# Performance work log

Hardware: AMD Instinct MI355X
Metric: run time of the kernel (lower is better)

## Reference

```python
import jax, jax.numpy as jnp
import numpy as np

B, NEG = 2, 16            # queries, negatives per query
N, E, D = 10000, 80000, 128  # nodes, edges, feature dim (in_dim == out_dim)
NUM_REL = 237
L = 3                     # PNA layers
NODE_RATIO = 0.1
K = max(1, int(NODE_RATIO * N))  # static top-k: every repeated graph has exactly N nodes
EPS = 1e-5


def _score(hidden, rel, lin_W, lin_b, m1_W, m1_b, m2_W, m2_b):
    heur = jnp.concatenate([hidden, rel], axis=-1) @ lin_W + lin_b
    x = heur * hidden
    h = jax.nn.relu(x @ m1_W + m1_b)
    return jnp.squeeze(h @ m2_W + m2_b, -1)


def _pna_conv(hidden, src, dst, emask, deg, pre_W, pre_b, post_W, post_b, out_W, out_b):
    """PNA layer with mean/max/min/std aggregators and identity/amplification/attenuation
    scalers, restricted to edges where emask is True. deg is the (clamped >=1) degree used
    by the scalers."""
    BN = hidden.shape[0]
    # message: pre-linear on [x_i (target), x_j (source)] per edge  -> (Erep, D)
    m = jnp.concatenate([hidden[dst], hidden[src]], axis=-1) @ pre_W + pre_b
    w = emask.astype(hidden.dtype)[:, None]
    cnt = jax.ops.segment_sum(emask.astype(hidden.dtype), dst, num_segments=BN)
    denom = jnp.maximum(cnt, 1.0)[:, None]
    s1 = jax.ops.segment_sum(m * w, dst, num_segments=BN)
    s2 = jax.ops.segment_sum(m * m * w, dst, num_segments=BN)
    mean = s1 / denom
    var = jax.nn.relu(s2 / denom - mean * mean)
    std = jnp.sqrt(var + EPS)
    has = (cnt > 0)[:, None]
    mx = jnp.where(has, jax.ops.segment_max(jnp.where(emask[:, None], m, -jnp.inf), dst, num_segments=BN), 0.0)
    mn = jnp.where(has, jax.ops.segment_min(jnp.where(emask[:, None], m, jnp.inf), dst, num_segments=BN), 0.0)
    agg = jnp.concatenate([mean, mx, mn, std], axis=-1)           # (BN, 4D)
    logd = jnp.log(deg + 1.0)                                     # deg >= 1 -> logd > 0
    avg_log = jnp.mean(logd)
    agg = jnp.concatenate([agg, agg * (logd / avg_log)[:, None], agg * (avg_log / logd)[:, None]], axis=-1)  # (BN, 12D)
    return (agg @ post_W + post_b) @ out_W + out_b


def _forward(h_index, r_index, t_index, hidden_states, edge_index, rel_embedding,
             lin_W, lin_b, m1_W, m1_b, m2_W, m2_b, pre_W, pre_b, post_W, post_b, out_W, out_b):
    sc = (lin_W, lin_b, m1_W, m1_b, m2_W, m2_b)
    # negative_sample_to_tail
    is_t_neg = jnp.all(h_index == h_index[:, :1], axis=-1, keepdims=True)
    h_idx = jnp.where(is_t_neg, h_index, t_index)
    t_idx = jnp.where(is_t_neg, t_index, h_index)
    r_idx = jnp.where(is_t_neg, r_index, r_index + NUM_REL)
    # repeat_graph
    offsets = jnp.arange(B, dtype=h_idx.dtype) * N               # (B,)
    src = jnp.tile(edge_index[0], B) + jnp.repeat(offsets, E)    # (B*E,)
    dst = jnp.tile(edge_index[1], B) + jnp.repeat(offsets, E)
    BN = B * N
    rel_embeds = rel_embedding[r_idx[:, 0]].astype(hidden_states.dtype)  # (B, D)
    flat_h = h_idx[:, 0] + offsets
    flat_t = t_idx[:, 0] + offsets
    # literal `repeat_interleave(N, dim=0)[:B]` quirk -> row arange(B)//N of gathered embs
    sel = jnp.arange(B) // N
    h_vals = hidden_states[h_idx[:, 0]][sel]                     # (B, D)
    t_vals = hidden_states[t_idx[:, 0]][sel]
    # init_input_embeds: boundary condition + initial score at head nodes
    boundary = jnp.zeros((BN, D), hidden_states.dtype).at[flat_t].set(t_vals).at[flat_h].set(h_vals)
    score = jnp.zeros(BN, jnp.float32).at[flat_h].set(_score(h_vals, rel_embeds, *sc))
    hidden = boundary
    rel_per_node = jnp.repeat(rel_embeds, N, axis=0)             # (BN, D), rel_embeds[batch_rep]
    rows = jnp.arange(B)[:, None]
    for l in range(L):
        # select_edges_pyg with degree_ratio=1.0: all out-edges of per-graph top-k nodes
        _, idx = jax.lax.top_k(score.reshape(B, N), K)           # (B, K)
        node_sel = jnp.zeros((B, N), bool).at[rows, idx].set(True).reshape(-1)
        emask = node_sel[src]                                    # (B*E,) selected-edge mask
        out_deg = jax.ops.segment_sum(emask.astype(jnp.float32), src, num_segments=BN)
        deg_sub = jnp.maximum(out_deg.astype(hidden.dtype), 1.0)
        new_hidden = _pna_conv(hidden, src, dst, emask, deg_sub,
                               pre_W[l], pre_b[l], post_W[l], post_b[l], out_W[l], out_b[l])
        # residual only for nodes with selected outgoing edges
        hidden = jnp.where((out_deg > 0)[:, None], hidden + new_hidden, hidden)
        score = _score(hidden, rel_per_node, *sc)
    # read out scores at (repeated) tail indices -> (B, NEG)
    return score[t_idx + offsets[:, None]]


def setup_inputs() -> dict:
    key = jax.random.key(0)
    ks = jax.random.split(key, 14)
    s = 0.05
    hi = jax.random.randint(ks[0], (B, 1), 0, N)
    h_index = jnp.tile(hi, (1, NEG))                 # constant per row (assert in forward)
    r0 = jax.random.randint(ks[1], (B, 1), 0, NUM_REL)
    r_index = jnp.tile(r0, (1, NEG))                 # constant per row (assert in forward)
    t_index = jax.random.randint(ks[2], (B, NEG), 0, N)
    hidden_states = jax.random.normal(ks[3], (N, D), jnp.float32)
    edge_index = jax.random.randint(ks[4], (2, E), 0, N)
    return {
        "h_index": h_index, "r_index": r_index, "t_index": t_index,
        "hidden_states": hidden_states, "edge_index": edge_index,
        "rel_embedding": jax.random.normal(ks[5], (2 * NUM_REL, D), jnp.float32) * s,
        "lin_W": jax.random.normal(ks[6], (2 * D, D), jnp.float32) * s, "lin_b": jnp.zeros(D, jnp.float32),
        "m1_W": jax.random.normal(ks[7], (D, D), jnp.float32) * s, "m1_b": jnp.zeros(D, jnp.float32),
        "m2_W": jax.random.normal(ks[8], (D, 1), jnp.float32) * s, "m2_b": jnp.zeros(1, jnp.float32),
        "pre_W": jax.random.normal(ks[9], (L, 2 * D, D), jnp.float32) * s, "pre_b": jnp.zeros((L, D), jnp.float32),
        "post_W": jax.random.normal(ks[10], (L, 12 * D, D), jnp.float32) * s, "post_b": jnp.zeros((L, D), jnp.float32),
        "out_W": jax.random.normal(ks[11], (L, D, D), jnp.float32) * s, "out_b": jnp.zeros((L, D), jnp.float32),
    }


def reference(h_index, r_index, t_index, hidden_states, edge_index, rel_embedding,
              lin_W, lin_b, m1_W, m1_b, m2_W, m2_b, pre_W, pre_b, post_W, post_b, out_W, out_b):
    return _forward(h_index, r_index, t_index, hidden_states, edge_index, rel_embedding,
                    lin_W, lin_b, m1_W, m1_b, m2_W, m2_b, pre_W, pre_b, post_W, post_b, out_W, out_b)
```

## Files before the change

kernel.cpp:

```cpp
#include <hip/hip_runtime.h>
#include <math.h>

#define Bq 2
#define NEG 16
#define Nn 10000
#define Ee 80000
#define Dd 128
#define NUM_REL 237
#define Ll 3
#define K_SEL 1000
#define BN (Bq*Nn)
#define EPSV 1e-5f
#define MAXACT 2048
#define MAXTOUCH 8192
#define SELCAP 3328
#define LN2F 0.69314718056f

constexpr size_t HID_OFF   = 0;
constexpr size_t SCORE_OFF = HID_OFF   + (size_t)BN*Dd*4;
constexpr size_t CVEC_OFF  = SCORE_OFF + (size_t)BN*4;
constexpr size_t HDR_OFF   = CVEC_OFF  + (size_t)Bq*Dd*4;
constexpr size_t THR_OFF   = HDR_OFF   + 64*4;
constexpr size_t INC_OFF   = THR_OFF   + Bq*8;
constexpr size_t DEG_OFF   = INC_OFF   + (size_t)BN*4;
constexpr size_t SLOT_OFF  = DEG_OFF   + (size_t)BN*4;
constexpr size_t CNT_OFF   = SLOT_OFF  + (size_t)BN*4;
constexpr size_t SDEG_OFF  = CNT_OFF   + (size_t)MAXACT*4;
constexpr size_t S1_OFF    = SDEG_OFF  + (size_t)MAXACT*4;
constexpr size_t S2_OFF    = S1_OFF    + (size_t)MAXACT*Dd*4;
constexpr size_t MXB_OFF   = S2_OFF    + (size_t)MAXACT*Dd*4;
constexpr size_t MNB_OFF   = MXB_OFF   + (size_t)MAXACT*Dd*4;
constexpr size_t TPART_OFF = MNB_OFF   + (size_t)MAXACT*Dd*4;
constexpr size_t ALIST_OFF = TPART_OFF + (size_t)4*MAXACT*Dd*4;
constexpr size_t FLAG_OFF  = ALIST_OFF + (size_t)MAXACT*4;
constexpr size_t TLIST_OFF = FLAG_OFF  + (size_t)BN*4;
constexpr size_t EDGE_OFF  = TLIST_OFF + (size_t)MAXTOUCH*4;
constexpr size_t CTR_OFF   = EDGE_OFF  + (size_t)Bq*Ee*2*4;

__device__ __forceinline__ unsigned encf(float f){
  unsigned u = __float_as_uint(f);
  return (u & 0x80000000u) ? ~u : (u | 0x80000000u);
}
__device__ __forceinline__ float decf(unsigned e){
  unsigned u = (e & 0x80000000u) ? (e & 0x7FFFFFFFu) : ~e;
  return __uint_as_float(u);
}
__device__ __forceinline__ unsigned long long make_key(float f, int i){
  unsigned d = ~encf(f);
  return ((unsigned long long)d << 32) | (unsigned)i;
}

__global__ __launch_bounds__(256) void k_init(
    const int* __restrict__ h_index, const int* __restrict__ r_index, const int* __restrict__ t_index,
    const float* __restrict__ hidden_states, const float* __restrict__ rel_embedding,
    const float* __restrict__ lin_W, const float* __restrict__ lin_b,
    const float* __restrict__ m1_W, const float* __restrict__ m1_b,
    const float* __restrict__ m2_W, const float* __restrict__ m2_b,
    int* __restrict__ hdr, float* __restrict__ cvec, float* __restrict__ hidden,
    float* __restrict__ score, unsigned* __restrict__ flag, int* __restrict__ tlist,
    unsigned* __restrict__ deg0, unsigned* __restrict__ ctr)
{
  __shared__ struct {
    int hbuf[Bq*NEG], tbuf[Bq*NEG], rbuf[Bq*NEG];
    int fh[Bq], ft[Bq], r0[Bq], eqf[Bq], hsrc, tsrc;
    float s0red[Dd]; float sc0;
    float relv[Bq][Dd], cv[Bq][Dd], hv[Dd], x[Bq][Dd], p[Bq][Dd];
  } sp;
  const int tid = threadIdx.x;
  const int bid = blockIdx.x;
  if (tid < Bq*NEG){
    sp.hbuf[tid] = h_index[tid];
    sp.tbuf[tid] = t_index[tid];
    sp.rbuf[tid] = r_index[tid];
  }
  if (tid < Dd) sp.s0red[tid] = fmaxf(m1_b[tid], 0.f) * m2_W[tid];
  __syncthreads();
  if (tid == 0){
    for (int b = 0; b < Bq; b++){
      bool eq = true;
      for (int j = 1; j < NEG; j++) eq = eq && (sp.hbuf[b*NEG+j] == sp.hbuf[b*NEG]);
      int h0 = eq ? sp.hbuf[b*NEG] : sp.tbuf[b*NEG];
      int t0 = eq ? sp.tbuf[b*NEG] : sp.hbuf[b*NEG];
      int r0 = eq ? sp.rbuf[b*NEG] : sp.rbuf[b*NEG] + NUM_REL;
      sp.fh[b] = h0 + b*Nn; sp.ft[b] = t0 + b*Nn;
      sp.r0[b] = r0; sp.eqf[b] = eq ? 1 : 0;
      if (b == 0){ sp.hsrc = h0; sp.tsrc = t0; }
    }
    float s = m2_b[0];
    for (int k = 0; k < Dd; k++) s += sp.s0red[k];
    sp.sc0 = s;
    if (bid == 0){
      ctr[4] = __float_as_uint(s);
      hdr[0] = sp.fh[0]; hdr[1] = sp.fh[1];
      hdr[2] = sp.ft[0]; hdr[3] = sp.ft[1];
      for (int b = 0; b < Bq; b++)
        for (int j = 0; j < NEG; j++){
          int tj = sp.eqf[b] ? sp.tbuf[b*NEG+j] : sp.hbuf[b*NEG+j];
          hdr[4 + b*NEG + j] = tj + b*Nn;
        }
      int cand[4] = { sp.ft[0], sp.fh[0], sp.ft[1], sp.fh[1] };
      int n = 0;
      for (int c = 0; c < 4; c++){
        bool dup = false;
        for (int m = 0; m < n; m++) dup = dup || (tlist[m] == cand[c]);
        if (!dup) tlist[n++] = cand[c];
        flag[cand[c]] = 1u;
      }
      ctr[3] = (unsigned)n;
    }
  }
  __syncthreads();
  const int fh0 = sp.fh[0], fh1 = sp.fh[1];
  const int ft0 = sp.ft[0], ft1 = sp.ft[1];
  const float sc0 = sp.sc0;
  if (bid == 0){
    int b = tid >> 7, d = tid & 127;
    sp.relv[b][d] = rel_embedding[(size_t)sp.r0[b]*Dd + d];
    if (b == 0) sp.hv[d] = hidden_states[(size_t)sp.hsrc*Dd + d];
    __syncthreads();
    float acc = lin_b[d];
    #pragma unroll 8
    for (int k = 0; k < Dd; k++) acc += sp.relv[b][k]*lin_W[(Dd+k)*Dd + d];
    sp.cv[b][d] = acc; cvec[b*Dd + d] = acc;
    hidden[(size_t)sp.ft[b]*Dd + d] = hidden_states[(size_t)sp.tsrc*Dd + d];
    hidden[(size_t)sp.fh[b]*Dd + d] = hidden_states[(size_t)sp.hsrc*Dd + d];
    __syncthreads();
    float hv = sp.hv[d];
    float heur = sp.cv[b][d];
    #pragma unroll 8
    for (int k = 0; k < Dd; k++) heur += sp.hv[k]*lin_W[k*Dd + d];
    sp.x[b][d] = heur * hv;
    __syncthreads();
    float a2 = m1_b[d];
    #pragma unroll 8
    for (int k = 0; k < Dd; k++) a2 += sp.x[b][k]*m1_W[k*Dd + d];
    sp.p[b][d] = fmaxf(a2, 0.f) * m2_W[d];
    __syncthreads();
    if (tid < Bq){
      float s = m2_b[0];
      for (int k = 0; k < Dd; k++) s += sp.p[tid][k];
      score[sp.fh[tid]] = s;
    }
  } else {
    int zb = bid - 1, znb = gridDim.x - 1;
    int zt = zb*256 + tid, zs = znb*256;
    float4 z4 = make_float4(0.f, 0.f, 0.f, 0.f);
    for (int i = zt; i < BN*32; i += zs){
      int row = i >> 5;
      if (row != ft0 && row != ft1 && row != fh0 && row != fh1)
        ((float4*)hidden)[i] = z4;
    }
    for (int v = zt; v < BN; v += zs){
      if (v != ft0 && v != ft1 && v != fh0 && v != fh1) flag[v] = 0u;
      if (v != fh0 && v != fh1) score[v] = sc0;
      if (v < Nn) deg0[v] = 0u;
    }
  }
}

__global__ __launch_bounds__(256) void k_selzero(
    const float* __restrict__ score, const int* __restrict__ tlist,
    unsigned long long* __restrict__ thr,
    float* __restrict__ s1, float* __restrict__ s2,
    unsigned* __restrict__ mxb, unsigned* __restrict__ mnb,
    unsigned* __restrict__ incnt, unsigned* __restrict__ ctr,
    const int* __restrict__ ei, unsigned* __restrict__ deg0, int do_deg0)
{
  int tid = threadIdx.x;
  int bid = blockIdx.x;
  if (bid < Bq){
    int b = bid;
    int nt = (int)ctr[3];
    unsigned d0 = ~encf(__uint_as_float(ctr[4]));
    __shared__ unsigned sd[SELCAP];
    __shared__ unsigned short sidx[SELCAP];
    __shared__ unsigned hist[256], histT[256];
    __shared__ int ntb_sh;
    __shared__ unsigned long long pref_sh;
    __shared__ unsigned kk_sh;
    if (tid == 0){ ntb_sh = 0; pref_sh = 0ull; kk_sh = K_SEL; }
    __syncthreads();
    int vlo = b*Nn, vhi = vlo + Nn;
    for (int i = tid; i < nt; i += 256){
      int v = tlist[i];
      if (v >= vlo && v < vhi){
        int pos = atomicAdd(&ntb_sh, 1);
        if (pos < SELCAP){
          sd[pos] = ~encf(score[v]);
          sidx[pos] = (unsigned short)(v - vlo);
        }
      }
    }
    __syncthreads();
    int ntb = min(ntb_sh, SELCAP);
    unsigned nvirt = (unsigned)(Nn - ntb);
    for (int pass = 7; pass >= 0; --pass){
      hist[tid] = 0u; histT[tid] = 0u;
      __syncthreads();
      unsigned long long pref = pref_sh;
      int sh_hi = 8*(pass+1);
      for (int j = tid; j < ntb; j += 256){
        unsigned long long key = ((unsigned long long)sd[j] << 32) | (unsigned long long)sidx[j];
        bool ok = (pass==7) || ((key >> sh_hi) == (pref >> sh_hi));
        if (ok) atomicAdd(&hist[(unsigned)(key >> (8*pass)) & 255u], 1u);
        if (pass < 4){
          unsigned idx = sidx[j];
          bool oki = (pass == 3) || ((idx >> sh_hi) == (((unsigned)pref) >> sh_hi));
          if (oki) atomicAdd(&histT[(idx >> (8*pass)) & 255u], 1u);
        }
      }
      __syncthreads();
      if (pass >= 4){
        if (tid == 0){
          unsigned long long keyv_hi = ((unsigned long long)d0 << 32);
          bool ok = (pass==7) || ((keyv_hi >> sh_hi) == (pref_sh >> sh_hi));
          if (ok) atomicAdd(&hist[(d0 >> (8*(pass-4))) & 255u], nvirt);
        }
      } else {
        if ((unsigned)(pref >> 32) == d0){
          unsigned long long hf = 0ull;
          if (pass < 3) hf = (unsigned long long)((((unsigned)pref) >> sh_hi)) << sh_hi;
          unsigned long long lo = hf + ((unsigned long long)tid << (8*pass));
          unsigned long long hi = lo + (1ull << (8*pass));
          unsigned long long nn = (unsigned long long)Nn;
          unsigned long long l2 = lo < nn ? lo : nn;
          unsigned long long h2 = hi < nn ? hi : nn;
          if (h2 > l2){
            unsigned c = (unsigned)(h2 - l2) - histT[tid];
            if (c > 0u) atomicAdd(&hist[tid], c);
          }
        }
      }
      __syncthreads();
      {
        unsigned kk = kk_sh;
        unsigned cum = 0;
        for (int i = 0; i < tid; i++) cum += hist[i];
        unsigned h = hist[tid];
        if (h > 0u && cum < kk && kk <= cum + h){
          pref_sh |= ((unsigned long long)tid) << (8*pass);
          kk_sh = kk - cum;
        }
      }
      __syncthreads();
    }
    if (tid == 0) thr[b] = pref_sh;
  } else {
    int zb = bid - Bq, znb = gridDim.x - Bq;
    int zt = zb*256 + tid, zs = znb*256;
    for (int i = zt; i < MAXACT*Dd; i += zs){
      s1[i] = 0.f; s2[i] = 0.f; mxb[i] = 0u; mnb[i] = 0xFFFFFFFFu;
    }
    for (int i = zt; i < BN; i += zs) incnt[i] = 0u;
    if (zt < 3) ctr[zt] = 0u;
    if (do_deg0){
      for (int e = zt; e < Ee; e += zs) atomicAdd(&deg0[ei[e]], 1u);
    }
  }
}

__global__ void k_build(const int* __restrict__ ei, const float* __restrict__ score,
                        const unsigned long long* __restrict__ thr,
                        const unsigned* __restrict__ deg0,
                        int* __restrict__ node_slot, int* __restrict__ alist,
                        float* __restrict__ slot_deg, unsigned* __restrict__ incnt,
                        int* __restrict__ edges, unsigned* __restrict__ ctr,
                        unsigned* __restrict__ flag, int* __restrict__ tlist){
  int i = blockIdx.x*blockDim.x + threadIdx.x;
  unsigned long long th0 = thr[0], th1 = thr[1];
  if (i < BN){
    int b = (i >= Nn) ? 1 : 0;
    int v0 = i - b*Nn;
    unsigned dg = deg0[v0];
    if (dg > 0u && make_key(score[i], v0) <= (b ? th1 : th0)){
      int slot = (int)atomicAdd(&ctr[0], 1u);
      alist[slot] = i; node_slot[i] = slot; slot_deg[slot] = (float)dg;
      atomicAdd((float*)&ctr[2], logf((float)dg + 1.0f));
      if (atomicExch(&flag[i], 1u) == 0u){
        int p = (int)atomicAdd(&ctr[3], 1u);
        tlist[p] = i;
      }
    }
  }
  if (i < Ee){
    int s0 = ei[i], d0e = ei[Ee + i];
    unsigned dgd = deg0[d0e];
    if (make_key(score[s0], s0) <= th0 && dgd > 0u && make_key(score[d0e], d0e) <= th0){
      int j = (int)atomicAdd(&ctr[1], 1u);
      edges[2*j] = s0; edges[2*j+1] = d0e;
      atomicAdd(&incnt[d0e], 1u);
    }
    int sv = s0 + Nn, dv = d0e + Nn;
    if (make_key(score[sv], s0) <= th1 && dgd > 0u && make_key(score[dv], d0e) <= th1){
      int j = (int)atomicAdd(&ctr[1], 1u);
      edges[2*j] = sv; edges[2*j+1] = dv;
      atomicAdd(&incnt[dv], 1u);
    }
  }
}

__global__ __launch_bounds__(256) void k_messages(
    const float* __restrict__ hidden, const int* __restrict__ edges,
    const int* __restrict__ node_slot,
    const float* __restrict__ preW, const float* __restrict__ preb,
    float* __restrict__ s1, float* __restrict__ s2,
    unsigned* __restrict__ mxb, unsigned* __restrict__ mnb,
    const unsigned* __restrict__ ctr){
  int ne = (int)ctr[1];
  int tid = threadIdx.x;
  int half = tid >> 7, d = tid & 127;
  __shared__ float sd[8][Dd], ss[8][Dd];
  float pb = preb[d];
  for (int j0 = blockIdx.x*8; j0 < ne; j0 += gridDim.x*8){
    int base = j0 + half*4;
    int nv = ne - base; if (nv > 4) nv = 4; if (nv < 0) nv = 0;
    int dsl[4];
    #pragma unroll
    for (int e = 0; e < 4; e++){
      int j = (e < nv) ? base + e : j0;
      int s = edges[2*j]; int dv = edges[2*j+1];
      dsl[e] = node_slot[dv];
      sd[half*4+e][d] = hidden[(size_t)dv*Dd + d];
      ss[half*4+e][d] = hidden[(size_t)s*Dd + d];
    }
    __syncthreads();
    float a[4] = {pb, pb, pb, pb};
    #pragma unroll 4
    for (int k = 0; k < Dd; k++){
      float w0 = preW[k*Dd + d];
      float w1 = preW[(Dd+k)*Dd + d];
      #pragma unroll
      for (int e = 0; e < 4; e++)
        a[e] += sd[half*4+e][k]*w0 + ss[half*4+e][k]*w1;
    }
    for (int e = 0; e < nv; e++){
      int dslot = dsl[e];
      atomicAdd(&s1[dslot*Dd + d], a[e]);
      atomicAdd(&s2[dslot*Dd + d], a[e]*a[e]);
      atomicMax(&mxb[dslot*Dd + d], encf(a[e]));
      atomicMin(&mnb[dslot*Dd + d], encf(a[e]));
    }
    __syncthreads();
  }
}

__global__ __launch_bounds__(512) void k_post(
    const unsigned* __restrict__ incnt, const int* __restrict__ alist,
    const float* __restrict__ s1, const float* __restrict__ s2,
    const unsigned* __restrict__ mxb, const unsigned* __restrict__ mnb,
    const float* __restrict__ slot_deg,
    const float* __restrict__ postW, float* __restrict__ tpart,
    const unsigned* __restrict__ ctr){
  int na = (int)ctr[0];
  int bid = blockIdx.x;
  int tile = bid & 63, ch = bid >> 6;
  if (tile*32 >= na) return;
  float logsum = __uint_as_float(ctr[2]);
  float avg = (logsum + (float)(BN - na)*LN2F) / (float)BN;
  __shared__ float lb[32*136];
  __shared__ float wbuf[3*16*128];
  __shared__ float sden[32];
  __shared__ unsigned shas[32];
  int tid = threadIdx.x;
  if (tid < 32){
    int slot = tile*32 + tid;
    unsigned c = (slot < na) ? incnt[alist[slot]] : 0u;
    sden[tid] = fmaxf((float)c, 1.0f);
    shas[tid] = c;
  }
  __syncthreads();
  for (int idx = tid; idx < 32*Dd; idx += 512){
    int sl = idx >> 7, kk = idx & 127;
    int gi = (tile*32 + sl)*Dd + kk;
    float den = sden[sl];
    float val;
    if (ch == 0)      val = s1[gi]/den;
    else if (ch == 1) val = shas[sl] ? decf(mxb[gi]) : 0.f;
    else if (ch == 2) val = shas[sl] ? decf(mnb[gi]) : 0.f;
    else {
      float mv = s1[gi]/den;
      float var = s2[gi]/den - mv*mv;
      val = sqrtf(fmaxf(var, 0.f) + EPSV);
    }
    lb[sl*136 + kk] = val;
  }
  int cg = tid & 31, rg = tid >> 5;
  int c0 = cg*4;
  float a0[2][4], a1[2][4], a2[2][4];
  #pragma unroll
  for (int i = 0; i < 2; i++)
    #pragma unroll
    for (int j = 0; j < 4; j++){ a0[i][j]=0.f; a1[i][j]=0.f; a2[i][j]=0.f; }
  for (int chunk = 0; chunk < 8; ++chunk){
    #pragma unroll
    for (int i = 0; i < 3; ++i){
      int f = tid + i*512;
      int q = f >> 9, r = f & 511;
      int kk = r >> 5, c4 = r & 31;
      int grow = q*512 + ch*128 + chunk*16 + kk;
      ((float4*)wbuf)[f] = *(const float4*)(postW + (size_t)grow*Dd + c4*4);
    }
    __syncthreads();
    #pragma unroll
    for (int k4 = 0; k4 < 4; ++k4){
      float4 av0 = *(const float4*)&lb[(rg*2+0)*136 + chunk*16 + k4*4];
      float4 av1 = *(const float4*)&lb[(rg*2+1)*136 + chunk*16 + k4*4];
      #pragma unroll
      for (int j = 0; j < 4; ++j){
        int kk = k4*4 + j;
        float4 w0 = *(const float4*)&wbuf[kk*128 + c0];
        float4 w1 = *(const float4*)&wbuf[(16+kk)*128 + c0];
        float4 w2 = *(const float4*)&wbuf[(32+kk)*128 + c0];
        float av[2] = { (&av0.x)[j], (&av1.x)[j] };
        #pragma unroll
        for (int i = 0; i < 2; i++){
          float a = av[i];
          a0[i][0] += a*w0.x; a0[i][1] += a*w0.y; a0[i][2] += a*w0.z; a0[i][3] += a*w0.w;
          a1[i][0] += a*w1.x; a1[i][1] += a*w1.y; a1[i][2] += a*w1.z; a1[i][3] += a*w1.w;
          a2[i][0] += a*w2.x; a2[i][1] += a*w2.y; a2[i][2] += a*w2.z; a2[i][3] += a*w2.w;
        }
      }
    }
    __syncthreads();
  }
  #pragma unroll
  for (int i = 0; i < 2; i++){
    int slot = tile*32 + rg*2 + i;
    if (slot < na){
      float dg = slot_deg[slot];
      float logd = logf(dg + 1.f);
      float al = logd/avg, be = avg/logd;
      float4 r;
      r.x = a0[i][0] + al*a1[i][0] + be*a2[i][0];
      r.y = a0[i][1] + al*a1[i][1] + be*a2[i][1];
      r.z = a0[i][2] + al*a1[i][2] + be*a2[i][2];
      r.w = a0[i][3] + al*a1[i][3] + be*a2[i][3];
      *(float4*)(tpart + (size_t)ch*MAXACT*Dd + (size_t)slot*Dd + c0) = r;
    }
  }
}

__global__ __launch_bounds__(256) void k_out_resid(
    const float* __restrict__ tpart, const int* __restrict__ alist,
    const float* __restrict__ outW, const float* __restrict__ outb,
    const float* __restrict__ postb, float* __restrict__ hidden,
    const unsigned* __restrict__ ctr){
  int na = (int)ctr[0];
  int tile = blockIdx.x;
  if (tile*32 >= na) return;
  __shared__ float tr[32*136];
  __shared__ float wbuf[16*128];
  int tid = threadIdx.x;
  for (int idx = tid; idx < 32*Dd; idx += 256){
    int sl = idx >> 7, kk = idx & 127;
    size_t o = (size_t)(tile*32 + sl)*Dd + kk;
    tr[sl*136 + kk] = tpart[o] + tpart[(size_t)MAXACT*Dd + o]
                    + tpart[(size_t)2*MAXACT*Dd + o] + tpart[(size_t)3*MAXACT*Dd + o]
                    + postb[kk];
  }
  int cg = tid & 31, rg = tid >> 5;
  int c0 = cg*4;
  float4 ob = *(const float4*)(outb + c0);
  float acc[4][4];
  #pragma unroll
  for (int r = 0; r < 4; r++){ acc[r][0]=ob.x; acc[r][1]=ob.y; acc[r][2]=ob.z; acc[r][3]=ob.w; }
  for (int chunk = 0; chunk < 8; ++chunk){
    #pragma unroll
    for (int i = 0; i < 2; ++i){
      int f = tid + i*256;
      int kk = f >> 5, c4 = f & 31;
      ((float4*)wbuf)[f] = *(const float4*)(outW + (size_t)(chunk*16 + kk)*Dd + c4*4);
    }
    __syncthreads();
    #pragma unroll
    for (int k4 = 0; k4 < 4; ++k4){
      float4 av[4];
      #pragma unroll
      for (int r = 0; r < 4; r++)
        av[r] = *(const float4*)&tr[(rg*4+r)*136 + chunk*16 + k4*4];
      #pragma unroll
      for (int j = 0; j < 4; ++j){
        float4 w = *(const float4*)&wbuf[(k4*4+j)*128 + c0];
        #pragma unroll
        for (int r = 0; r < 4; r++){
          float a = (&av[r].x)[j];
          acc[r][0] += a*w.x; acc[r][1] += a*w.y; acc[r][2] += a*w.z; acc[r][3] += a*w.w;
        }
      }
    }
    __syncthreads();
  }
  #pragma unroll
  for (int r = 0; r < 4; r++){
    int slot = tile*32 + rg*4 + r;
    if (slot < na){
      int v = alist[slot];
      float* hp = hidden + (size_t)v*Dd + c0;
      float4 h4 = *(float4*)hp;
      h4.x += acc[r][0]; h4.y += acc[r][1]; h4.z += acc[r][2]; h4.w += acc[r][3];
      *(float4*)hp = h4;
    }
  }
}

__global__ __launch_bounds__(256) void k_score(
    const float* __restrict__ hidden, const float* __restrict__ cvec,
    const float* __restrict__ linW,
    const float* __restrict__ m1W, const float* __restrict__ m1b,
    const float* __restrict__ m2W, const float* __restrict__ m2b,
    const int* __restrict__ tlist, const unsigned* __restrict__ ctr,
    float* __restrict__ score,
    const int* __restrict__ ovr, int ovr_n, float* __restrict__ outp){
  int nt = (ovr_n > 0) ? ovr_n : (int)ctr[3];
  const int* list = (ovr_n > 0) ? ovr : tlist;
  int nb = blockIdx.x * 32;
  if (nb >= nt) return;
  __shared__ float sh[32*Dd];
  __shared__ float sx[32*Dd];
  __shared__ float sc[2*Dd];
  __shared__ int   sv[32];
  __shared__ float red[32*33];
  int tid = threadIdx.x;
  if (tid < 32){
    int idx = nb + tid;
    sv[tid] = (idx < nt) ? list[idx] : list[nb];
  }
  sc[tid] = cvec[tid];
  __syncthreads();
  for (int q = tid; q < 32*32; q += 256){
    int row = q >> 5, f4 = q & 31;
    ((float4*)sh)[row*32 + f4] = ((const float4*)(hidden + (size_t)sv[row]*Dd))[f4];
  }
  __syncthreads();
  int cg = tid & 31, rg = tid >> 5;
  int c0 = cg*4;
  float acc[4][4];
  #pragma unroll
  for (int i = 0; i < 4; i++){ acc[i][0]=0.f; acc[i][1]=0.f; acc[i][2]=0.f; acc[i][3]=0.f; }
  for (int k4 = 0; k4 < 32; k4++){
    float4 av[4];
    #pragma unroll
    for (int i = 0; i < 4; i++) av[i] = ((float4*)sh)[(rg*4+i)*32 + k4];
    #pragma unroll
    for (int j = 0; j < 4; j++){
      float4 w = *(const float4*)(linW + (size_t)(k4*4+j)*Dd + c0);
      #pragma unroll
      for (int i = 0; i < 4; i++){
        float a = (&av[i].x)[j];
        acc[i][0] += a*w.x; acc[i][1] += a*w.y; acc[i][2] += a*w.z; acc[i][3] += a*w.w;
      }
    }
  }
  #pragma unroll
  for (int i = 0; i < 4; i++){
    int row = rg*4 + i;
    int bb = (sv[row] >= Nn) ? 1 : 0;
    float4 cv = *(float4*)&sc[bb*Dd + c0];
    float4 hv = ((float4*)sh)[row*32 + cg];
    float4 x;
    x.x = (acc[i][0] + cv.x)*hv.x;
    x.y = (acc[i][1] + cv.y)*hv.y;
    x.z = (acc[i][2] + cv.z)*hv.z;
    x.w = (acc[i][3] + cv.w)*hv.w;
    ((float4*)sx)[row*32 + cg] = x;
  }
  __syncthreads();
  #pragma unroll
  for (int i = 0; i < 4; i++){ acc[i][0]=0.f; acc[i][1]=0.f; acc[i][2]=0.f; acc[i][3]=0.f; }
  for (int k4 = 0; k4 < 32; k4++){
    float4 av[4];
    #pragma unroll
    for (int i = 0; i < 4; i++) av[i] = ((float4*)sx)[(rg*4+i)*32 + k4];
    #pragma unroll
    for (int j = 0; j < 4; j++){
      float4 w = *(const float4*)(m1W + (size_t)(k4*4+j)*Dd + c0);
      #pragma unroll
      for (int i = 0; i < 4; i++){
        float a = (&av[i].x)[j];
        acc[i][0] += a*w.x; acc[i][1] += a*w.y; acc[i][2] += a*w.z; acc[i][3] += a*w.w;
      }
    }
  }
  float4 mb = *(const float4*)(m1b + c0);
  float4 mw = *(const float4*)(m2W + c0);
  #pragma unroll
  for (int i = 0; i < 4; i++){
    float p0 = fmaxf(acc[i][0]+mb.x, 0.f)*mw.x;
    float p1 = fmaxf(acc[i][1]+mb.y, 0.f)*mw.y;
    float p2 = fmaxf(acc[i][2]+mb.z, 0.f)*mw.z;
    float p3 = fmaxf(acc[i][3]+mb.w, 0.f)*mw.w;
    red[(rg*4+i)*33 + cg] = p0+p1+p2+p3;
  }
  __syncthreads();
  if (tid < 32){
    float s = m2b[0];
    for (int g = 0; g < 32; g++) s += red[tid*33 + g];
    if (nb + tid < nt){
      if (ovr_n > 0) outp[nb + tid] = s;
      else           score[sv[tid]] = s;
    }
  }
}

extern "C" void kernel_launch(void* const* d_in, const int* in_sizes, int n_in,
                              void* d_out, int out_size, void* d_ws, size_t ws_size,
                              hipStream_t stream){
  const int*   h_index       = (const int*)d_in[0];
  const int*   r_index       = (const int*)d_in[1];
  const int*   t_index       = (const int*)d_in[2];
  const float* hidden_states = (const float*)d_in[3];
  const int*   edge_index    = (const int*)d_in[4];
  const float* rel_embedding = (const float*)d_in[5];
  const float* lin_W  = (const float*)d_in[6];
  const float* lin_b  = (const float*)d_in[7];
  const float* m1_W   = (const float*)d_in[8];
  const float* m1_b   = (const float*)d_in[9];
  const float* m2_W   = (const float*)d_in[10];
  const float* m2_b   = (const float*)d_in[11];
  const float* pre_W  = (const float*)d_in[12];
  const float* pre_b  = (const float*)d_in[13];
  const float* post_W = (const float*)d_in[14];
  const float* post_b = (const float*)d_in[15];
  const float* out_W  = (const float*)d_in[16];
  const float* out_b  = (const float*)d_in[17];

  char* ws = (char*)d_ws;
  float*    hidden   = (float*)(ws + HID_OFF);
  float*    score    = (float*)(ws + SCORE_OFF);
  float*    cvec     = (float*)(ws + CVEC_OFF);
  int*      hdr      = (int*)(ws + HDR_OFF);
  unsigned long long* thr = (unsigned long long*)(ws + THR_OFF);
  unsigned* incnt    = (unsigned*)(ws + INC_OFF);
  unsigned* deg0     = (unsigned*)(ws + DEG_OFF);
  int*      node_slot= (int*)(ws + SLOT_OFF);
  float*    slot_deg = (float*)(ws + SDEG_OFF);
  float*    s1       = (float*)(ws + S1_OFF);
  float*    s2       = (float*)(ws + S2_OFF);
  unsigned* mxb      = (unsigned*)(ws + MXB_OFF);
  unsigned* mnb      = (unsigned*)(ws + MNB_OFF);
  float*    tpart    = (float*)(ws + TPART_OFF);
  int*      alist    = (int*)(ws + ALIST_OFF);
  unsigned* flag     = (unsigned*)(ws + FLAG_OFF);
  int*      tlist    = (int*)(ws + TLIST_OFF);
  int*      edges    = (int*)(ws + EDGE_OFF);
  unsigned* ctr      = (unsigned*)(ws + CTR_OFF);

  k_init<<<416, 256, 0, stream>>>(h_index, r_index, t_index, hidden_states, rel_embedding,
                                  lin_W, lin_b, m1_W, m1_b, m2_W, m2_b,
                                  hdr, cvec, hidden, score, flag, tlist, deg0, ctr);
  for (int l = 0; l < Ll; ++l){
    const float* preWl  = pre_W  + (size_t)l*2*Dd*Dd;
    const float* prebl  = pre_b  + (size_t)l*Dd;
    const float* postWl = post_W + (size_t)l*12*Dd*Dd;
    const float* postbl = post_b + (size_t)l*Dd;
    const float* outWl  = out_W  + (size_t)l*Dd*Dd;
    const float* outbl  = out_b  + (size_t)l*Dd;

    k_selzero<<<130, 256, 0, stream>>>(score, tlist, thr, s1, s2, mxb, mnb,
                                       incnt, ctr, edge_index, deg0, (l == 0) ? 1 : 0);
    k_build<<<(Ee + 255)/256, 256, 0, stream>>>(edge_index, score, thr, deg0,
                                                node_slot, alist, slot_deg, incnt,
                                                edges, ctr, flag, tlist);
    k_messages<<<384, 256, 0, stream>>>(hidden, edges, node_slot, preWl, prebl,
                                        s1, s2, mxb, mnb, ctr);
    k_post<<<256, 512, 0, stream>>>(incnt, alist, s1, s2, mxb, mnb, slot_deg,
                                    postWl, tpart, ctr);
    k_out_resid<<<MAXACT/32, 256, 0, stream>>>(tpart, alist, outWl, outbl, postbl,
                                               hidden, ctr);
    if (l < Ll-1){
      k_score<<<MAXTOUCH/32, 256, 0, stream>>>(hidden, cvec, lin_W, m1_W, m1_b, m2_W, m2_b,
                                               tlist, ctr, score, tlist, 0, score);
    } else {
      k_score<<<1, 256, 0, stream>>>(hidden, cvec, lin_W, m1_W, m1_b, m2_W, m2_b,
                                     tlist, ctr, score, hdr + 4, Bq*NEG, (float*)d_out);
    }
  }
}
```

Measured before the change: 433.3 us.

## Fuse rescoring into output/residual kernel and aggregate build atomics per wavefront

The separate scoring pass over all touched nodes after each layer is folded into the output-projection/residual kernel, which now scores the updated active nodes directly from registers via a shared-memory union. A small extra scoring launch after layer 0 covers the head nodes. In k_build, global atomic counters are replaced by wavefront ballot/popcount compaction, and the log-degree sum is reduced per block in shared memory before one global atomic. This cuts kernel launches, re-reads of hidden rows and global atomic contention, but changes which nodes get rescored (active set instead of the touched list), which may matter for correctness.

New measurement: 457.0 us. 1.05x slower.

```diff
diff --git a/kernel.cpp b/kernel.cpp
--- a/kernel.cpp
+++ b/kernel.cpp
@@ -267,36 +267,80 @@
                         int* __restrict__ edges, unsigned* __restrict__ ctr,
                         unsigned* __restrict__ flag, int* __restrict__ tlist){
   int i = blockIdx.x*blockDim.x + threadIdx.x;
+  int lane = threadIdx.x & 63;
+  unsigned long long lmask = (1ull << lane) - 1ull;
   unsigned long long th0 = thr[0], th1 = thr[1];
-  if (i < BN){
+  __shared__ float blog;
+  if (threadIdx.x == 0) blog = 0.f;
+  __syncthreads();
+  {
+    bool pn = false; unsigned dg = 0;
     int b = (i >= Nn) ? 1 : 0;
     int v0 = i - b*Nn;
-    unsigned dg = deg0[v0];
-    if (dg > 0u && make_key(score[i], v0) <= (b ? th1 : th0)){
-      int slot = (int)atomicAdd(&ctr[0], 1u);
-      alist[slot] = i; node_slot[i] = slot; slot_deg[slot] = (float)dg;
-      atomicAdd((float*)&ctr[2], logf((float)dg + 1.0f));
-      if (atomicExch(&flag[i], 1u) == 0u){
-        int p = (int)atomicAdd(&ctr[3], 1u);
-        tlist[p] = i;
-      }
-    }
-  }
-  if (i < Ee){
-    int s0 = ei[i], d0e = ei[Ee + i];
-    unsigned dgd = deg0[d0e];
-    if (make_key(score[s0], s0) <= th0 && dgd > 0u && make_key(score[d0e], d0e) <= th0){
-      int j = (int)atomicAdd(&ctr[1], 1u);
-      edges[2*j] = s0; edges[2*j+1] = d0e;
-      atomicAdd(&incnt[d0e], 1u);
-    }
-    int sv = s0 + Nn, dv = d0e + Nn;
-    if (make_key(score[sv], s0) <= th1 && dgd > 0u && make_key(score[dv], d0e) <= th1){
-      int j = (int)atomicAdd(&ctr[1], 1u);
-      edges[2*j] = sv; edges[2*j+1] = dv;
-      atomicAdd(&incnt[dv], 1u);
-    }
-  }
+    if (i < BN){
+      dg = deg0[v0];
+      pn = (dg > 0u) && (make_key(score[i], v0) <= (b ? th1 : th0));
+    }
+    unsigned long long mn_ = __ballot(pn);
+    if (mn_ != 0ull){
+      int lead = __ffsll((unsigned long long)mn_) - 1;
+      int base = 0;
+      if (lane == lead) base = (int)atomicAdd(&ctr[0], (unsigned)__popcll(mn_));
+      base = __shfl(base, lead);
+      if (pn){
+        int slot = base + __popcll(mn_ & lmask);
+        alist[slot] = i; node_slot[i] = slot; slot_deg[slot] = (float)dg;
+        atomicAdd(&blog, logf((float)dg + 1.0f));
+      }
+    }
+    bool newt = false;
+    if (pn) newt = (atomicExch(&flag[i], 1u) == 0u);
+    unsigned long long mt = __ballot(newt);
+    if (mt != 0ull){
+      int lead = __ffsll((unsigned long long)mt) - 1;
+      int base = 0;
+      if (lane == lead) base = (int)atomicAdd(&ctr[3], (unsigned)__popcll(mt));
+      base = __shfl(base, lead);
+      if (newt) tlist[base + __popcll(mt & lmask)] = i;
+    }
+  }
+  {
+    bool pe0 = false, pe1 = false; int s0 = 0, d0e = 0;
+    if (i < Ee){
+      s0 = ei[i]; d0e = ei[Ee + i];
+      unsigned dgd = deg0[d0e];
+      if (dgd > 0u){
+        pe0 = (make_key(score[s0], s0) <= th0) && (make_key(score[d0e], d0e) <= th0);
+        pe1 = (make_key(score[s0 + Nn], s0) <= th1) && (make_key(score[d0e + Nn], d0e) <= th1);
+      }
+    }
+    unsigned long long m0 = __ballot(pe0);
+    if (m0 != 0ull){
+      int lead = __ffsll((unsigned long long)m0) - 1;
+      int base = 0;
+      if (lane == lead) base = (int)atomicAdd(&ctr[1], (unsigned)__popcll(m0));
+      base = __shfl(base, lead);
+      if (pe0){
+        int j = base + __popcll(m0 & lmask);
+        edges[2*j] = s0; edges[2*j+1] = d0e;
+        atomicAdd(&incnt[d0e], 1u);
+      }
+    }
+    unsigned long long m1 = __ballot(pe1);
+    if (m1 != 0ull){
+      int lead = __ffsll((unsigned long long)m1) - 1;
+      int base = 0;
+      if (lane == lead) base = (int)atomicAdd(&ctr[1], (unsigned)__popcll(m1));
+      base = __shfl(base, lead);
+      if (pe1){
+        int j = base + __popcll(m1 & lmask);
+        edges[2*j] = s0 + Nn; edges[2*j+1] = d0e + Nn;
+        atomicAdd(&incnt[d0e + Nn], 1u);
+      }
+    }
+  }
+  __syncthreads();
+  if (threadIdx.x == 0 && blog != 0.f) atomicAdd((float*)&ctr[2], blog);
 }
 
 __global__ __launch_bounds__(256) void k_messages(
@@ -440,23 +484,29 @@
   }
 }
 
-__global__ __launch_bounds__(256) void k_out_resid(
+__global__ __launch_bounds__(256) void k_out_score(
     const float* __restrict__ tpart, const int* __restrict__ alist,
     const float* __restrict__ outW, const float* __restrict__ outb,
     const float* __restrict__ postb, float* __restrict__ hidden,
-    const unsigned* __restrict__ ctr){
+    const unsigned* __restrict__ ctr,
+    const float* __restrict__ cvec, const float* __restrict__ linW,
+    const float* __restrict__ m1W, const float* __restrict__ m1b,
+    const float* __restrict__ m2W, const float* __restrict__ m2b,
+    float* __restrict__ score, int do_score){
   int na = (int)ctr[0];
   int tile = blockIdx.x;
   if (tile*32 >= na) return;
-  __shared__ float tr[32*136];
-  __shared__ float wbuf[16*128];
+  __shared__ union {
+    struct { float tr[32*136]; float wbuf[16*128]; } p1;
+    struct { float sh[32*Dd]; float sx[32*Dd]; float sc[2*Dd]; float red[32*33]; } p2;
+  } sm;
   int tid = threadIdx.x;
   for (int idx = tid; idx < 32*Dd; idx += 256){
     int sl = idx >> 7, kk = idx & 127;
     size_t o = (size_t)(tile*32 + sl)*Dd + kk;
-    tr[sl*136 + kk] = tpart[o] + tpart[(size_t)MAXACT*Dd + o]
-                    + tpart[(size_t)2*MAXACT*Dd + o] + tpart[(size_t)3*MAXACT*Dd + o]
-                    + postb[kk];
+    sm.p1.tr[sl*136 + kk] = tpart[o] + tpart[(size_t)MAXACT*Dd + o]
+                          + tpart[(size_t)2*MAXACT*Dd + o] + tpart[(size_t)3*MAXACT*Dd + o]
+                          + postb[kk];
   }
   int cg = tid & 31, rg = tid >> 5;
   int c0 = cg*4;
@@ -469,7 +519,7 @@
     for (int i = 0; i < 2; ++i){
       int f = tid + i*256;
       int kk = f >> 5, c4 = f & 31;
-      ((float4*)wbuf)[f] = *(const float4*)(outW + (size_t)(chunk*16 + kk)*Dd + c4*4);
+      ((float4*)sm.p1.wbuf)[f] = *(const float4*)(outW + (size_t)(chunk*16 + kk)*Dd + c4*4);
     }
     __syncthreads();
     #pragma unroll
@@ -477,10 +527,10 @@
       float4 av[4];
       #pragma unroll
       for (int r = 0; r < 4; r++)
-        av[r] = *(const float4*)&tr[(rg*4+r)*136 + chunk*16 + k4*4];
+        av[r] = *(const float4*)&sm.p1.tr[(rg*4+r)*136 + chunk*16 + k4*4];
       #pragma unroll
       for (int j = 0; j < 4; ++j){
-        float4 w = *(const float4*)&wbuf[(k4*4+j)*128 + c0];
+        float4 w = *(const float4*)&sm.p1.wbuf[(k4*4+j)*128 + c0];
         #pragma unroll
         for (int r = 0; r < 4; r++){
           float a = (&av[r].x)[j];
@@ -490,15 +540,92 @@
     }
     __syncthreads();
   }
+  float4 h4s[4];
   #pragma unroll
   for (int r = 0; r < 4; r++){
     int slot = tile*32 + rg*4 + r;
+    h4s[r] = make_float4(0.f, 0.f, 0.f, 0.f);
     if (slot < na){
       int v = alist[slot];
       float* hp = hidden + (size_t)v*Dd + c0;
       float4 h4 = *(float4*)hp;
       h4.x += acc[r][0]; h4.y += acc[r][1]; h4.z += acc[r][2]; h4.w += acc[r][3];
       *(float4*)hp = h4;
+      h4s[r] = h4;
+    }
+  }
+  if (!do_score) return;
+  __syncthreads();
+  sm.p2.sc[tid] = cvec[tid];
+  #pragma unroll
+  for (int r = 0; r < 4; r++)
+    *(float4*)&sm.p2.sh[(rg*4+r)*Dd + c0] = h4s[r];
+  __syncthreads();
+  float ac2[4][4];
+  #pragma unroll
+  for (int i = 0; i < 4; i++){ ac2[i][0]=0.f; ac2[i][1]=0.f; ac2[i][2]=0.f; ac2[i][3]=0.f; }
+  for (int k4 = 0; k4 < 32; k4++){
+    float4 av[4];
+    #pragma unroll
+    for (int i = 0; i < 4; i++) av[i] = ((float4*)sm.p2.sh)[(rg*4+i)*32 + k4];
+    #pragma unroll
+    for (int j = 0; j < 4; j++){
+      float4 w = *(const float4*)(linW + (size_t)(k4*4+j)*Dd + c0);
+      #pragma unroll
+      for (int i = 0; i < 4; i++){
+        float a = (&av[i].x)[j];
+        ac2[i][0] += a*w.x; ac2[i][1] += a*w.y; ac2[i][2] += a*w.z; ac2[i][3] += a*w.w;
+      }
+    }
+  }
+  #pragma unroll
+  for (int i = 0; i < 4; i++){
+    int row = rg*4 + i;
+    int slot = tile*32 + row;
+    int bb = (alist[slot] >= Nn) ? 1 : 0;
+    float4 cv = *(float4*)&sm.p2.sc[bb*Dd + c0];
+    float4 hv = ((float4*)sm.p2.sh)[row*32 + cg];
+    float4 x;
+    x.x = (ac2[i][0] + cv.x)*hv.x;
+    x.y = (ac2[i][1] + cv.y)*hv.y;
+    x.z = (ac2[i][2] + cv.z)*hv.z;
+    x.w = (ac2[i][3] + cv.w)*hv.w;
+    ((float4*)sm.p2.sx)[row*32 + cg] = x;
+  }
+  __syncthreads();
+  #pragma unroll
+  for (int i = 0; i < 4; i++){ ac2[i][0]=0.f; ac2[i][1]=0.f; ac2[i][2]=0.f; ac2[i][3]=0.f; }
+  for (int k4 = 0; k4 < 32; k4++){
+    float4 av[4];
+    #pragma unroll
+    for (int i = 0; i < 4; i++) av[i] = ((float4*)sm.p2.sx)[(rg*4+i)*32 + k4];
+    #pragma unroll
+    for (int j = 0; j < 4; j++){
+      float4 w = *(const float4*)(m1W + (size_t)(k4*4+j)*Dd + c0);
+      #pragma unroll
+      for (int i = 0; i < 4; i++){
+        float a = (&av[i].x)[j];
+        ac2[i][0] += a*w.x; ac2[i][1] += a*w.y; ac2[i][2] += a*w.z; ac2[i][3] += a*w.w;
+      }
+    }
+  }
+  float4 mb = *(const float4*)(m1b + c0);
+  float4 mw = *(const float4*)(m2W + c0);
+  #pragma unroll
+  for (int i = 0; i < 4; i++){
+    float p0 = fmaxf(ac2[i][0]+mb.x, 0.f)*mw.x;
+    float p1 = fmaxf(ac2[i][1]+mb.y, 0.f)*mw.y;
+    float p2 = fmaxf(ac2[i][2]+mb.z, 0.f)*mw.z;
+    float p3 = fmaxf(ac2[i][3]+mb.w, 0.f)*mw.w;
+    sm.p2.red[(rg*4+i)*33 + cg] = p0+p1+p2+p3;
+  }
+  __syncthreads();
+  if (tid < 32){
+    int slot = tile*32 + tid;
+    if (slot < na){
+      float s = m2b[0];
+      for (int g = 0; g < 32; g++) s += sm.p2.red[tid*33 + g];
+      score[alist[slot]] = s;
     }
   }
 }
@@ -508,23 +635,15 @@
     const float* __restrict__ linW,
     const float* __restrict__ m1W, const float* __restrict__ m1b,
     const float* __restrict__ m2W, const float* __restrict__ m2b,
-    const int* __restrict__ tlist, const unsigned* __restrict__ ctr,
-    float* __restrict__ score,
-    const int* __restrict__ ovr, int ovr_n, float* __restrict__ outp){
-  int nt = (ovr_n > 0) ? ovr_n : (int)ctr[3];
-  const int* list = (ovr_n > 0) ? ovr : tlist;
-  int nb = blockIdx.x * 32;
-  if (nb >= nt) return;
+    const int* __restrict__ list, int nt, float* __restrict__ outp,
+    float* __restrict__ score_arr, int to_score){
   __shared__ float sh[32*Dd];
   __shared__ float sx[32*Dd];
   __shared__ float sc[2*Dd];
   __shared__ int   sv[32];
   __shared__ float red[32*33];
   int tid = threadIdx.x;
-  if (tid < 32){
-    int idx = nb + tid;
-    sv[tid] = (idx < nt) ? list[idx] : list[nb];
-  }
+  if (tid < 32) sv[tid] = (tid < nt) ? list[tid] : list[0];
   sc[tid] = cvec[tid];
   __syncthreads();
   for (int q = tid; q < 32*32; q += 256){
@@ -595,9 +714,9 @@
   if (tid < 32){
     float s = m2b[0];
     for (int g = 0; g < 32; g++) s += red[tid*33 + g];
-    if (nb + tid < nt){
-      if (ovr_n > 0) outp[nb + tid] = s;
-      else           score[sv[tid]] = s;
+    if (tid < nt){
+      if (to_score) score_arr[sv[tid]] = s;
+      else          outp[tid] = s;
     }
   }
 }
@@ -665,14 +784,15 @@
                                         s1, s2, mxb, mnb, ctr);
     k_post<<<256, 512, 0, stream>>>(incnt, alist, s1, s2, mxb, mnb, slot_deg,
                                     postWl, tpart, ctr);
-    k_out_resid<<<MAXACT/32, 256, 0, stream>>>(tpart, alist, outWl, outbl, postbl,
-                                               hidden, ctr);
-    if (l < Ll-1){
-      k_score<<<MAXTOUCH/32, 256, 0, stream>>>(hidden, cvec, lin_W, m1_W, m1_b, m2_W, m2_b,
-                                               tlist, ctr, score, tlist, 0, score);
-    } else {
+    k_out_score<<<MAXACT/32, 256, 0, stream>>>(tpart, alist, outWl, outbl, postbl,
+                                               hidden, ctr, cvec, lin_W,
+                                               m1_W, m1_b, m2_W, m2_b,
+                                               score, (l < Ll-1) ? 1 : 0);
+    if (l == 0){
       k_score<<<1, 256, 0, stream>>>(hidden, cvec, lin_W, m1_W, m1_b, m2_W, m2_b,
-                                     tlist, ctr, score, hdr + 4, Bq*NEG, (float*)d_out);
-    }
-  }
-}
+                                     hdr, 4, (float*)d_out, score, 1);
+    }
+  }
+  k_score<<<1, 256, 0, stream>>>(hidden, cvec, lin_W, m1_W, m1_b, m2_W, m2_b,
+                                 hdr + 4, Bq*NEG, (float*)d_out, score, 0);
+}
```
